# Performance work log

Measured on AMD Instinct MI355X. Metric: run time of the kernel, lower is better.

Reference implementation:

```python
import jax, jax.numpy as jnp
import numpy as np


def setup_inputs() -> dict:
    key = jax.random.key(0)
    k1, k2, k3, k4 = jax.random.split(key, 4)
    N, S, F, UNITS = 50000, 32, 128, 128
    x = jax.random.normal(k1, (N, F), dtype=jnp.float32)
    neigh_x = jax.random.normal(k2, (N, S, F), dtype=jnp.float32)
    kernel_self = jax.random.normal(k3, (F, UNITS), dtype=jnp.float32) * 0.05
    kernel_neigh = jax.random.normal(k4, (F, UNITS), dtype=jnp.float32) * 0.05
    bias = jnp.zeros((2 * UNITS,), dtype=jnp.float32)
    return {"x": x, "neigh_x": neigh_x, "kernel_self": kernel_self,
            "kernel_neigh": kernel_neigh, "bias": bias}


def reference(x, neigh_x, kernel_self, kernel_neigh, bias):
    # neigh_x: [N, S, F]. Original transposes to [N, F, S] and applies
    # tf.raw_ops.NthElement with n = S//2 + S%2 (n-th smallest, 0-indexed)
    # along the last (neighbor) axis. Equivalent: sort along neighbor axis
    # of the untransposed tensor and take index n.
    S = neigh_x.shape[1]
    n = S // 2 + S % 2
    med = jnp.sort(neigh_x, axis=1)[:, n, :]  # [N, F]
    out = jnp.concatenate([x @ kernel_self, med @ kernel_neigh], axis=1)  # [N, 2*units] (concat=True)
    out = out + bias
    return jax.nn.relu(out)
```

## Files before the change

### kernel.cpp

```cpp
#include <hip/hip_runtime.h>

namespace {

constexpr int S   = 32;
constexpr int F   = 128;
constexpr int BR  = 32;
constexpr int TPB = 256;

__global__ __launch_bounds__(TPB) void fused_median_gemm(
    const float* __restrict__ x,
    const float* __restrict__ neigh,
    const float* __restrict__ Ks,
    const float* __restrict__ Kn,
    const float* __restrict__ bias,
    float* __restrict__ out,
    int N)
{
    __shared__ __align__(16) float xs[BR][F];
    __shared__ __align__(16) float ms[BR][F];

    const int tid  = threadIdx.x;
    const int row0 = blockIdx.x * BR;

    {
        const int f  = tid & (F - 1);
        const int rp = tid >> 7;
#pragma unroll 1
        for (int i = 0; i < BR; i += 2) {
            const int rl = i + rp;
            int row = row0 + rl;
            if (row > N - 1) row = N - 1;
            const float* base = neigh + (size_t)row * (S * F) + f;
            float v[S];
#pragma unroll
            for (int s = 0; s < S; ++s) v[s] = base[(size_t)s * F];

#pragma unroll
            for (int k = 2; k <= S; k <<= 1) {
#pragma unroll
                for (int j = k >> 1; j > 0; j >>= 1) {
#pragma unroll
                    for (int a = 0; a < S; ++a) {
                        const int b = a ^ j;
                        if (b > a) {
                            const bool up = (a & k) == 0;
                            const float lo = fminf(v[a], v[b]);
                            const float hi = fmaxf(v[a], v[b]);
                            v[a] = up ? lo : hi;
                            v[b] = up ? hi : lo;
                        }
                    }
                }
            }
            ms[rl][f] = v[16];
            xs[rl][f] = x[(size_t)row * F + f];
        }
    }
    __syncthreads();

    const int tu   = tid & 31;
    const int tr   = tid >> 5;
    const int ucol = tu * 8;
    const bool self_half = (tu < 16);
    const float* __restrict__ W = self_half ? Ks : Kn;
    const int ul = self_half ? ucol : (ucol - 128);
    const float* lin = self_half ? &xs[0][0] : &ms[0][0];

    float4 acc[4][2];
#pragma unroll
    for (int r = 0; r < 4; ++r) {
        acc[r][0] = float4{0.f, 0.f, 0.f, 0.f};
        acc[r][1] = float4{0.f, 0.f, 0.f, 0.f};
    }

    for (int f0 = 0; f0 < F; f0 += 4) {
        float4 wv[4][2];
#pragma unroll
        for (int df = 0; df < 4; ++df) {
            wv[df][0] = *(const float4*)&W[(f0 + df) * 128 + ul];
            wv[df][1] = *(const float4*)&W[(f0 + df) * 128 + ul + 4];
        }
        float4 xv[4];
#pragma unroll
        for (int r = 0; r < 4; ++r)
            xv[r] = *(const float4*)&lin[(tr * 4 + r) * F + f0];

#pragma unroll
        for (int r = 0; r < 4; ++r) {
            const float xc[4] = {xv[r].x, xv[r].y, xv[r].z, xv[r].w};
#pragma unroll
            for (int df = 0; df < 4; ++df) {
#pragma unroll
                for (int h = 0; h < 2; ++h) {
                    acc[r][h].x = fmaf(xc[df], wv[df][h].x, acc[r][h].x);
                    acc[r][h].y = fmaf(xc[df], wv[df][h].y, acc[r][h].y);
                    acc[r][h].z = fmaf(xc[df], wv[df][h].z, acc[r][h].z);
                    acc[r][h].w = fmaf(xc[df], wv[df][h].w, acc[r][h].w);
                }
            }
        }
    }

    const float4 bv0 = *(const float4*)&bias[ucol];
    const float4 bv1 = *(const float4*)&bias[ucol + 4];
#pragma unroll
    for (int r = 0; r < 4; ++r) {
        const int row = row0 + tr * 4 + r;
        if (row < N) {
            float4 o0, o1;
            o0.x = fmaxf(acc[r][0].x + bv0.x, 0.f);
            o0.y = fmaxf(acc[r][0].y + bv0.y, 0.f);
            o0.z = fmaxf(acc[r][0].z + bv0.z, 0.f);
            o0.w = fmaxf(acc[r][0].w + bv0.w, 0.f);
            o1.x = fmaxf(acc[r][1].x + bv1.x, 0.f);
            o1.y = fmaxf(acc[r][1].y + bv1.y, 0.f);
            o1.z = fmaxf(acc[r][1].z + bv1.z, 0.f);
            o1.w = fmaxf(acc[r][1].w + bv1.w, 0.f);
            *(float4*)&out[(size_t)row * 256 + ucol]     = o0;
            *(float4*)&out[(size_t)row * 256 + ucol + 4] = o1;
        }
    }
}

}

extern "C" void kernel_launch(void* const* d_in, const int* in_sizes, int n_in,
                              void* d_out, int out_size, void* d_ws, size_t ws_size,
                              hipStream_t stream) {
    const float* x     = (const float*)d_in[0];
    const float* neigh = (const float*)d_in[1];
    const float* Ks    = (const float*)d_in[2];
    const float* Kn    = (const float*)d_in[3];
    const float* bias  = (const float*)d_in[4];
    float* out = (float*)d_out;

    const int N = in_sizes[0] / F;
    const int grid = (N + BR - 1) / BR;
    hipLaunchKernelGGL(fused_median_gemm, dim3(grid), dim3(TPB), 0, stream,
                       x, neigh, Ks, Kn, bias, out, N);
}
```

Before: 203.2 us.

## Replace bitonic sort with Batcher 16-sorts plus merge-select median on float2

Computes the median by sorting two 16-element halves with an odd-even merge network and selecting the rank-16 element as min over max(A[q],B[15-q]), instead of a full 32-element bitonic sort. Each thread now handles two features via float2 loads, and neighbor loads and output stores use nontemporal hints. A minimum-blocks launch bound is added. This cuts ALU work in the selection phase so the kernel approaches the memory bound, at the cost of higher register pressure per thread.

```diff
diff --git a/kernel.cpp b/kernel.cpp
--- a/kernel.cpp
+++ b/kernel.cpp
@@ -1,13 +1,64 @@
 #include <hip/hip_runtime.h>
 
 namespace {
+
+typedef float f32x2 __attribute__((ext_vector_type(2)));
+typedef float f32x4 __attribute__((ext_vector_type(4)));
 
 constexpr int S   = 32;
 constexpr int F   = 128;
 constexpr int BR  = 32;
 constexpr int TPB = 256;
 
-__global__ __launch_bounds__(TPB) void fused_median_gemm(
+struct CEPair { int a, b; };
+
+constexpr int batcher_count16() {
+  int n = 16, cnt = 0;
+  for (int p = 1; p < n; p <<= 1)
+    for (int k = p; k >= 1; k >>= 1)
+      for (int j = k % p; j + k < n; j += 2 * k)
+        for (int i = 0; i < k && i + j + k < n; ++i)
+          if ((i + j) / (2 * p) == (i + j + k) / (2 * p))
+            ++cnt;
+  return cnt;
+}
+constexpr int NCE = batcher_count16();
+
+struct Net16 { CEPair ce[NCE]; };
+
+constexpr Net16 make_net16() {
+  Net16 net{};
+  int n = 16, c = 0;
+  for (int p = 1; p < n; p <<= 1)
+    for (int k = p; k >= 1; k >>= 1)
+      for (int j = k % p; j + k < n; j += 2 * k)
+        for (int i = 0; i < k && i + j + k < n; ++i)
+          if ((i + j) / (2 * p) == (i + j + k) / (2 * p))
+            net.ce[c++] = CEPair{i + j, i + j + k};
+  return net;
+}
+constexpr Net16 NET16 = make_net16();
+
+__device__ __forceinline__ f32x2 min2(f32x2 a, f32x2 b) {
+  f32x2 r; r.x = fminf(a.x, b.x); r.y = fminf(a.y, b.y); return r;
+}
+__device__ __forceinline__ f32x2 max2(f32x2 a, f32x2 b) {
+  f32x2 r; r.x = fmaxf(a.x, b.x); r.y = fmaxf(a.y, b.y); return r;
+}
+
+template<int T>
+__device__ __forceinline__ void sort16(f32x2 (&v)[16]) {
+  if constexpr (T < NCE) {
+    constexpr int a = NET16.ce[T].a;
+    constexpr int b = NET16.ce[T].b;
+    f32x2 x = v[a], y = v[b];
+    v[a] = min2(x, y);
+    v[b] = max2(x, y);
+    sort16<T + 1>(v);
+  }
+}
+
+__global__ __launch_bounds__(TPB, 4) void fused_median_gemm(
     const float* __restrict__ x,
     const float* __restrict__ neigh,
     const float* __restrict__ Ks,
@@ -23,37 +74,38 @@
     const int row0 = blockIdx.x * BR;
 
     {
-        const int f  = tid & (F - 1);
-        const int rp = tid >> 7;
+        const int lane = tid & 63;
+        const int rp   = tid >> 6;
 #pragma unroll 1
-        for (int i = 0; i < BR; i += 2) {
+        for (int i = 0; i < BR; i += 4) {
             const int rl = i + rp;
             int row = row0 + rl;
             if (row > N - 1) row = N - 1;
-            const float* base = neigh + (size_t)row * (S * F) + f;
-            float v[S];
+            const f32x2* base =
+                (const f32x2*)(neigh + (size_t)row * (S * F)) + lane;
+
+            f32x2 A[16], B[16];
 #pragma unroll
-            for (int s = 0; s < S; ++s) v[s] = base[(size_t)s * F];
+            for (int s = 0; s < 16; ++s)
+                A[s] = __builtin_nontemporal_load(base + (size_t)s * 64);
+#pragma unroll
+            for (int s = 0; s < 16; ++s)
+                B[s] = __builtin_nontemporal_load(base + (size_t)(16 + s) * 64);
 
+            sort16<0>(A);
+            sort16<0>(B);
+
+            f32x2 c[16];
 #pragma unroll
-            for (int k = 2; k <= S; k <<= 1) {
+            for (int q = 0; q < 16; ++q) c[q] = max2(A[q], B[15 - q]);
 #pragma unroll
-                for (int j = k >> 1; j > 0; j >>= 1) {
+            for (int st = 8; st >= 1; st >>= 1)
 #pragma unroll
-                    for (int a = 0; a < S; ++a) {
-                        const int b = a ^ j;
-                        if (b > a) {
-                            const bool up = (a & k) == 0;
-                            const float lo = fminf(v[a], v[b]);
-                            const float hi = fmaxf(v[a], v[b]);
-                            v[a] = up ? lo : hi;
-                            v[b] = up ? hi : lo;
-                        }
-                    }
-                }
-            }
-            ms[rl][f] = v[16];
-            xs[rl][f] = x[(size_t)row * F + f];
+                for (int q = 0; q < st; ++q) c[q] = min2(c[q], c[q + st]);
+
+            ((f32x2*)&ms[rl][0])[lane] = c[0];
+            ((f32x2*)&xs[rl][0])[lane] =
+                *((const f32x2*)(x + (size_t)row * F) + lane);
         }
     }
     __syncthreads();
@@ -66,48 +118,48 @@
     const int ul = self_half ? ucol : (ucol - 128);
     const float* lin = self_half ? &xs[0][0] : &ms[0][0];
 
-    float4 acc[4][2];
+    f32x4 acc[4][2];
 #pragma unroll
     for (int r = 0; r < 4; ++r) {
-        acc[r][0] = float4{0.f, 0.f, 0.f, 0.f};
-        acc[r][1] = float4{0.f, 0.f, 0.f, 0.f};
+        acc[r][0] = f32x4{0.f, 0.f, 0.f, 0.f};
+        acc[r][1] = f32x4{0.f, 0.f, 0.f, 0.f};
     }
 
     for (int f0 = 0; f0 < F; f0 += 4) {
-        float4 wv[4][2];
+        f32x4 wv[4][2];
 #pragma unroll
         for (int df = 0; df < 4; ++df) {
-            wv[df][0] = *(const float4*)&W[(f0 + df) * 128 + ul];
-            wv[df][1] = *(const float4*)&W[(f0 + df) * 128 + ul + 4];
+            wv[df][0] = *(const f32x4*)&W[(f0 + df) * 128 + ul];
+            wv[df][1] = *(const f32x4*)&W[(f0 + df) * 128 + ul + 4];
         }
-        float4 xv[4];
+        f32x4 xv[4];
 #pragma unroll
         for (int r = 0; r < 4; ++r)
-            xv[r] = *(const float4*)&lin[(tr * 4 + r) * F + f0];
+            xv[r] = *(const f32x4*)&lin[(tr * 4 + r) * F + f0];
 
 #pragma unroll
         for (int r = 0; r < 4; ++r) {
-            const float xc[4] = {xv[r].x, xv[r].y, xv[r].z, xv[r].w};
 #pragma unroll
             for (int df = 0; df < 4; ++df) {
+                const float xc = xv[r][df];
 #pragma unroll
                 for (int h = 0; h < 2; ++h) {
-                    acc[r][h].x = fmaf(xc[df], wv[df][h].x, acc[r][h].x);
-                    acc[r][h].y = fmaf(xc[df], wv[df][h].y, acc[r][h].y);
-                    acc[r][h].z = fmaf(xc[df], wv[df][h].z, acc[r][h].z);
-                    acc[r][h].w = fmaf(xc[df], wv[df][h].w, acc[r][h].w);
+                    acc[r][h].x = fmaf(xc, wv[df][h].x, acc[r][h].x);
+                    acc[r][h].y = fmaf(xc, wv[df][h].y, acc[r][h].y);
+                    acc[r][h].z = fmaf(xc, wv[df][h].z, acc[r][h].z);
+                    acc[r][h].w = fmaf(xc, wv[df][h].w, acc[r][h].w);
                 }
             }
         }
     }
 
-    const float4 bv0 = *(const float4*)&bias[ucol];
-    const float4 bv1 = *(const float4*)&bias[ucol + 4];
+    const f32x4 bv0 = *(const f32x4*)&bias[ucol];
+    const f32x4 bv1 = *(const f32x4*)&bias[ucol + 4];
 #pragma unroll
     for (int r = 0; r < 4; ++r) {
         const int row = row0 + tr * 4 + r;
         if (row < N) {
-            float4 o0, o1;
+            f32x4 o0, o1;
             o0.x = fmaxf(acc[r][0].x + bv0.x, 0.f);
             o0.y = fmaxf(acc[r][0].y + bv0.y, 0.f);
             o0.z = fmaxf(acc[r][0].z + bv0.z, 0.f);
@@ -116,8 +168,8 @@
             o1.y = fmaxf(acc[r][1].y + bv1.y, 0.f);
             o1.z = fmaxf(acc[r][1].z + bv1.z, 0.f);
             o1.w = fmaxf(acc[r][1].w + bv1.w, 0.f);
-            *(float4*)&out[(size_t)row * 256 + ucol]     = o0;
-            *(float4*)&out[(size_t)row * 256 + ucol + 4] = o1;
+            __builtin_nontemporal_store(o0, (f32x4*)&out[(size_t)row * 256 + ucol]);
+            __builtin_nontemporal_store(o1, (f32x4*)&out[(size_t)row * 256 + ucol + 4]);
         }
     }
 }
```

After: 197.0 us. 3.1% less time.
